# Kernel optimization log

Hardware: AMD Instinct MI355X
Metric: run time of the kernel (lower is better)

The kernel has to match this reference:

```python
import jax, jax.numpy as jnp
import numpy as np


def setup_inputs() -> dict:
    key = jax.random.key(0)
    kz, kh, k0 = jax.random.split(key, 3)
    B, C, D, H, W = 2, 96, 32, 32, 32
    z = jax.random.uniform(kz, (B, C, D, H, W), dtype=jnp.float32)  # gate in [0,1]
    h_tilde = jax.random.normal(kh, (B, C, D, H, W), dtype=jnp.float32)  # candidate state
    h0 = jax.random.uniform(k0, (1,), dtype=jnp.float32)  # scalar initial state
    return {"z": z, "h_tilde": h_tilde, "h0": h0}


def reference(z, h_tilde, h0):
    """GruDirection3d with d1=d2=d3=1 (forward_3, no flips).

    The three wavefront slice-updates in the torch code jointly implement
        out[d, y, x] = z[d, y, x] * h_tilde[d, y, x]
                       + (1 - z[d, y, x]) * out[d-1, y-1, x-1]
    with out == h0 whenever any index goes below 0 (the padded border).
    We realize it as t_num = min(D, H, W) full-volume shifted updates: after
    iteration k, all voxels with min(d, y, x) <= k-1 hold their final value,
    so after t_num iterations the result matches the torch wavefront DP exactly.
    """
    B, C, D, H, W = z.shape
    t_num = min(D, H, W)  # static shapes -> python int, jit-safe
    # padded state: index 0 along each spatial axis is the h0 border (never written)
    h_pad = jnp.full((B, C, D + 1, H + 1, W + 1), h0[0], dtype=z.dtype)

    one = jnp.asarray(1, dtype=z.dtype)

    def step(h_pad, _):
        prev = h_pad[:, :, :-1, :-1, :-1]  # out[d-1, y-1, x-1] (with border = h0)
        new = z * h_tilde + (one - z) * prev
        return h_pad.at[:, :, 1:, 1:, 1:].set(new), None

    h_pad, _ = jax.lax.scan(step, h_pad, None, length=t_num)
    return h_pad[:, :, 1:, 1:, 1:]
```

## Files before the change

kernel.cpp:

```cpp
#include <hip/hip_runtime.h>


#define PLANE 1024
#define DD 32

#define LDS_BARRIER()                                        \
    do {                                                     \
        asm volatile("s_waitcnt lgkmcnt(0)" ::: "memory");   \
        __builtin_amdgcn_s_barrier();                        \
    } while (0)

__global__ __launch_bounds__(1024) void gru3d_rawbar(
    const float* __restrict__ z,
    const float* __restrict__ ht,
    const float* __restrict__ h0p,
    float* __restrict__ out)
{
    __shared__ float buf[2][PLANE];

    const int bc  = blockIdx.x;
    const int tid = threadIdx.x;
    const int y   = tid >> 5;
    const int x   = tid & 31;

    const float* zb = z   + (size_t)bc * (DD * PLANE);
    const float* tb = ht  + (size_t)bc * (DD * PLANE);
    float*       ob = out + (size_t)bc * (DD * PLANE);

    const float h0 = h0p[0];

    float zr[DD], tr[DD];
    #pragma unroll
    for (int d = 0; d < DD; ++d) {
        zr[d] = zb[d * PLANE + tid];
        tr[d] = tb[d * PLANE + tid];
    }

    const bool interior = (y > 0) & (x > 0);

    float h = zr[0] * (tr[0] - h0) + h0;
    ob[tid] = h;
    buf[0][tid] = h;
    LDS_BARRIER();

    #pragma unroll
    for (int d = 1; d < DD; ++d) {
        const float pv = interior ? buf[(d - 1) & 1][tid - 33] : h0;
        const float hn = zr[d] * (tr[d] - pv) + pv;
        ob[d * PLANE + tid] = hn;
        buf[d & 1][tid] = hn;
        LDS_BARRIER();
    }
}

extern "C" void kernel_launch(void* const* d_in, const int* in_sizes, int n_in,
                              void* d_out, int out_size, void* d_ws, size_t ws_size,
                              hipStream_t stream) {
    const float* z  = (const float*)d_in[0];
    const float* ht = (const float*)d_in[1];
    const float* h0 = (const float*)d_in[2];
    float* out      = (float*)d_out;

    const int BC = 2 * 96;
    gru3d_rawbar<<<dim3(BC), dim3(1024), 0, stream>>>(z, ht, h0, out);
}
```

Before: 96.06 us.

## Vectorize GRU wavefront to float4 with 256 threads and rolling prefetch ring

Each thread now handles four adjacent x positions using float4 global and LDS accesses, so the block shrinks from 1024 to 256 threads. Instead of loading all 32 depth planes into registers up front, it keeps an 8-deep prefetch ring of z and h_tilde planes that is refilled as the depth recurrence advances. The aim is cheaper per-step barriers with fewer waves, fewer memory instructions, and load latency overlapped with the serial chain. The cost is less thread-level parallelism per block and extra shuffling for the diagonal neighbour, which straddles float4 lanes.

```diff
diff --git a/kernel.cpp b/kernel.cpp
--- a/kernel.cpp
+++ b/kernel.cpp
@@ -2,7 +2,8 @@
 
 
 #define PLANE 1024
-#define DD 32
+#define DD    32
+#define PF    8
 
 #define LDS_BARRIER()                                        \
     do {                                                     \
@@ -10,18 +11,20 @@
         __builtin_amdgcn_s_barrier();                        \
     } while (0)
 
-__global__ __launch_bounds__(1024) void gru3d_rawbar(
+__global__ __launch_bounds__(256) void gru3d_vec4(
     const float* __restrict__ z,
     const float* __restrict__ ht,
     const float* __restrict__ h0p,
     float* __restrict__ out)
 {
-    __shared__ float buf[2][PLANE];
+    __shared__ float hbuf[2][PLANE];
 
     const int bc  = blockIdx.x;
     const int tid = threadIdx.x;
-    const int y   = tid >> 5;
-    const int x   = tid & 31;
+    const int y   = tid >> 3;
+    const int xg  = tid & 7;
+    const int x0  = xg << 2;
+    const int off0 = y * 32 + x0;
 
     const float* zb = z   + (size_t)bc * (DD * PLANE);
     const float* tb = ht  + (size_t)bc * (DD * PLANE);
@@ -29,26 +32,57 @@
 
     const float h0 = h0p[0];
 
-    float zr[DD], tr[DD];
+    float4 zr[PF], tr[PF];
     #pragma unroll
-    for (int d = 0; d < DD; ++d) {
-        zr[d] = zb[d * PLANE + tid];
-        tr[d] = tb[d * PLANE + tid];
+    for (int p = 0; p < PF; ++p) {
+        zr[p] = *reinterpret_cast<const float4*>(zb + p * PLANE + off0);
+        tr[p] = *reinterpret_cast<const float4*>(tb + p * PLANE + off0);
     }
 
-    const bool interior = (y > 0) & (x > 0);
+    float4 h;
 
-    float h = zr[0] * (tr[0] - h0) + h0;
-    ob[tid] = h;
-    buf[0][tid] = h;
-    LDS_BARRIER();
+    {
+        const float4 zv = zr[0], tv = tr[0];
+        h.x = zv.x * (tv.x - h0) + h0;
+        h.y = zv.y * (tv.y - h0) + h0;
+        h.z = zv.z * (tv.z - h0) + h0;
+        h.w = zv.w * (tv.w - h0) + h0;
+        *reinterpret_cast<float4*>(&hbuf[0][off0]) = h;
+        *reinterpret_cast<float4*>(ob + off0) = h;
+        zr[0] = *reinterpret_cast<const float4*>(zb + PF * PLANE + off0);
+        tr[0] = *reinterpret_cast<const float4*>(tb + PF * PLANE + off0);
+        LDS_BARRIER();
+    }
 
     #pragma unroll
     for (int d = 1; d < DD; ++d) {
-        const float pv = interior ? buf[(d - 1) & 1][tid - 33] : h0;
-        const float hn = zr[d] * (tr[d] - pv) + pv;
-        ob[d * PLANE + tid] = hn;
-        buf[d & 1][tid] = hn;
+        const int s  = d & (PF - 1);
+        const int pb = (d - 1) & 1;
+        const float4 zv = zr[s], tv = tr[s];
+
+        float pv0, pv1, pv2, pv3;
+        if (y == 0) {
+            pv0 = pv1 = pv2 = pv3 = h0;
+        } else {
+            const float4 q = *reinterpret_cast<const float4*>(&hbuf[pb][off0 - 32]);
+            pv1 = q.x; pv2 = q.y; pv3 = q.z;
+            const int il = (off0 - 33 < 0) ? 0 : (off0 - 33);
+            const float left = hbuf[pb][il];
+            pv0 = (x0 > 0) ? left : h0;
+        }
+
+        h.x = zv.x * (tv.x - pv0) + pv0;
+        h.y = zv.y * (tv.y - pv1) + pv1;
+        h.z = zv.z * (tv.z - pv2) + pv2;
+        h.w = zv.w * (tv.w - pv3) + pv3;
+
+        *reinterpret_cast<float4*>(&hbuf[d & 1][off0]) = h;
+        *reinterpret_cast<float4*>(ob + d * PLANE + off0) = h;
+
+        if (d + PF < DD) {
+            zr[s] = *reinterpret_cast<const float4*>(zb + (d + PF) * PLANE + off0);
+            tr[s] = *reinterpret_cast<const float4*>(tb + (d + PF) * PLANE + off0);
+        }
         LDS_BARRIER();
     }
 }
@@ -62,5 +96,5 @@
     float* out      = (float*)d_out;
 
     const int BC = 2 * 96;
-    gru3d_rawbar<<<dim3(BC), dim3(1024), 0, stream>>>(z, ht, h0, out);
+    gru3d_vec4<<<dim3(BC), dim3(256), 0, stream>>>(z, ht, h0, out);
 }
```

New measurement: 95.94 us. No clear change (-0.1%).
